# Kernel optimization log

Measured on AMD Instinct MI355X. Metric: run time of the kernel, lower is better.

Reference implementation:

```python
import jax, jax.numpy as jnp
import numpy as np

N_NODES = 100000
N_EDGES = 1600000
N_GRAPHS = 512
IN_CH = 128
FILT = 128
N_CONVS = 4  # 1 + n_rounds(3)


def setup_inputs() -> dict:
    key = jax.random.key(0)
    ks = jax.random.split(key, 10)
    x = jax.random.normal(ks[0], (N_NODES, IN_CH), dtype=jnp.float32)
    edge_index = jax.random.randint(ks[1], (2, N_EDGES), 0, N_NODES, dtype=jnp.int32)
    batch = jnp.sort(jax.random.randint(ks[2], (N_NODES,), 0, N_GRAPHS, dtype=jnp.int32))
    # GCNConv weights (in_channels == filter_size so all convs stack uniformly)
    s = 1.0 / np.sqrt(FILT)
    conv_w = jax.random.uniform(ks[3], (N_CONVS, IN_CH, FILT), jnp.float32, -s, s)
    conv_b = jnp.zeros((N_CONVS, FILT), jnp.float32)
    fc1_w = jax.random.uniform(ks[4], (FILT, FILT), jnp.float32, -s, s)
    fc1_b = jax.random.uniform(ks[5], (FILT,), jnp.float32, -s, s)
    fc2_w = jax.random.uniform(ks[6], (FILT, 1), jnp.float32, -s, s)
    fc2_b = jax.random.uniform(ks[7], (1,), jnp.float32, -s, s)
    return {"x": x, "edge_index": edge_index, "batch": batch, "batch_size": N_GRAPHS,
            "conv_w": conv_w, "conv_b": conv_b,
            "fc1_w": fc1_w, "fc1_b": fc1_b, "fc2_w": fc2_w, "fc2_b": fc2_b}


def _gcn_layer(x, W, b, src, dst, dinv):
    # GCNConv with improved=True: A_hat = A + 2I, sym-normalized by D_hat^{-1/2}
    h = x @ W                                   # [N, F]
    enorm = dinv[src] * dinv[dst]               # [E]
    agg = jax.ops.segment_sum(h[src] * enorm[:, None], dst, num_segments=N_NODES)
    self_loop = (2.0 * dinv * dinv)[:, None] * h
    return agg + self_loop + b


def reference(x, edge_index, batch, batch_size, conv_w, conv_b, fc1_w, fc1_b, fc2_w, fc2_b):
    src, dst = edge_index[0], edge_index[1]
    # degree including improved self-loop weight 2
    deg = jax.ops.segment_sum(jnp.ones((N_EDGES,), x.dtype), dst, num_segments=N_NODES) + 2.0
    dinv = jax.lax.rsqrt(deg)
    for i in range(N_CONVS):
        x = _gcn_layer(x, conv_w[i], conv_b[i], src, dst, dinv)
        x = jax.nn.relu(x)
        # dropout is identity in eval mode
    # global mean pool over graphs
    sums = jax.ops.segment_sum(x, batch, num_segments=batch_size)
    cnt = jax.ops.segment_sum(jnp.ones((N_NODES,), x.dtype), batch, num_segments=batch_size)
    pooled = sums / jnp.maximum(cnt, 1.0)[:, None]   # [G, F]
    h = jax.nn.relu(pooled @ fc1_w + fc1_b)
    out = h @ fc2_w + fc2_b                          # [G, 1]
    return out[:, 0]
```

## Files before the change

### kernel.cpp

```cpp
#include <hip/hip_runtime.h>
#include <hip/hip_fp16.h>

#define N_NODES 100000
#define N_EDGES 1600000
#define N_GRAPHS 512
#define F 128
#define N_CONVS 4
#define SCAN_NBLK ((N_NODES + 1023) / 1024)
#define FILL_BLOCKS ((N_EDGES + 255) / 256)
#define NWIN 8
#define WIN_SZ ((N_NODES + NWIN - 1) / NWIN)

#define W2_STRIDE 132
#define W2_LAYER (128 * W2_STRIDE)

typedef __attribute__((ext_vector_type(8))) short short8;
typedef __attribute__((ext_vector_type(4))) float f32x4;

union FragU { uint4 u; short8 v; };
union HU4 { uint4 u; __half2 h[4]; };

__device__ __forceinline__ float4 fma4(float w, float4 v, float4 a) {
    a.x = fmaf(w, v.x, a.x); a.y = fmaf(w, v.y, a.y);
    a.z = fmaf(w, v.z, a.z); a.w = fmaf(w, v.w, a.w);
    return a;
}

__device__ __forceinline__ unsigned int pack_hilo(float f) {
    unsigned int u = __float_as_uint(f);
    unsigned int hb = u & 0xFFFF0000u;
    float d = f - __uint_as_float(hb);
    unsigned int lb = __float_as_uint(d) >> 16;
    return (u >> 16) | (lb << 16);
}


__global__ void count_kernel(const int* __restrict__ dst, int* __restrict__ cnt) {
    int e = blockIdx.x * blockDim.x + threadIdx.x;
    if (e < N_EDGES) atomicAdd(&cnt[dst[e]], 1);
}

__global__ void dinv_kernel(const int* __restrict__ cnt, float* __restrict__ dinv) {
    int n = blockIdx.x * blockDim.x + threadIdx.x;
    if (n < N_NODES) dinv[n] = rsqrtf((float)cnt[n] + 2.0f);
}

__global__ void scan1_kernel(const int* __restrict__ cnt, int* __restrict__ excl,
                             int* __restrict__ blksum) {
    __shared__ int sums[256];
    int t = threadIdx.x;
    int base = blockIdx.x * 1024 + t * 4;
    int v0 = 0, v1 = 0, v2 = 0, v3 = 0;
    if (base + 0 < N_NODES) v0 = cnt[base + 0];
    if (base + 1 < N_NODES) v1 = cnt[base + 1];
    if (base + 2 < N_NODES) v2 = cnt[base + 2];
    if (base + 3 < N_NODES) v3 = cnt[base + 3];
    int s = v0 + v1 + v2 + v3;
    sums[t] = s;
    __syncthreads();
    for (int off = 1; off < 256; off <<= 1) {
        int y = (t >= off) ? sums[t - off] : 0;
        __syncthreads();
        sums[t] += y;
        __syncthreads();
    }
    int pre = sums[t] - s;
    if (base + 0 < N_NODES) excl[base + 0] = pre;
    if (base + 1 < N_NODES) excl[base + 1] = pre + v0;
    if (base + 2 < N_NODES) excl[base + 2] = pre + v0 + v1;
    if (base + 3 < N_NODES) excl[base + 3] = pre + v0 + v1 + v2;
    if (t == 255) blksum[blockIdx.x] = sums[255];
}

__global__ void scan2_kernel(int* __restrict__ blksum, int nblk) {
    __shared__ int sh[128];
    int t = threadIdx.x;
    int v = (t < nblk) ? blksum[t] : 0;
    sh[t] = v;
    __syncthreads();
    for (int off = 1; off < 128; off <<= 1) {
        int y = (t >= off) ? sh[t - off] : 0;
        __syncthreads();
        sh[t] += y;
        __syncthreads();
    }
    if (t < nblk) blksum[t] = sh[t] - v;
}

__global__ void scan3_kernel(int* __restrict__ rowptr, const int* __restrict__ blksum,
                             int* __restrict__ fill) {
    int t = threadIdx.x;
    int base = blockIdx.x * 1024 + t * 4;
    int off = blksum[blockIdx.x];
#pragma unroll
    for (int i = 0; i < 4; i++) {
        int idx = base + i;
        if (idx < N_NODES) {
            int v = rowptr[idx] + off;
            rowptr[idx] = v;
            fill[idx] = v;
        }
    }
    if (blockIdx.x == 0 && t == 0) rowptr[N_NODES] = N_EDGES;
}


__global__ __launch_bounds__(256) void fillw_kernel(
        const int* __restrict__ src, const int* __restrict__ dst,
        const float* __restrict__ dinv, int* __restrict__ fill,
        int2* __restrict__ edges) {
    int b = blockIdx.x;
    int w = b & (NWIN - 1);
    int e = (b >> 3) * 256 + threadIdx.x;
    if (e < N_EDGES) {
        int d = dst[e];
        if (d / WIN_SZ == w) {
            int s = src[e];
            int pos = atomicAdd(&fill[d], 1);
            edges[pos] = make_int2(s, __float_as_int(dinv[s] * dinv[d]));
        }
    }
}


__global__ void wpack_kernel(const float* __restrict__ conv_w, unsigned int* __restrict__ W2g) {
    int idx = blockIdx.x * 256 + threadIdx.x;
    if (idx < N_CONVS * 16384) {
        int L = idx >> 14;
        int e = idx & 16383;
        int k = e >> 7;
        int n = e & 127;
        float f = conv_w[(size_t)L * 16384 + k * 128 + n];
        W2g[(size_t)L * W2_LAYER + n * W2_STRIDE + k] = pack_hilo(f);
    }
}


__global__ __launch_bounds__(256, 2) void gemm_mfma_kernel(const float* __restrict__ X,
                                                           const unsigned int* __restrict__ W2g,
                                                           __half* __restrict__ Hh) {
    __shared__ unsigned int wlds[128 * W2_STRIDE];
    int t = threadIdx.x;

    {
        const uint4* s4 = (const uint4*)W2g;
        uint4* d4 = (uint4*)wlds;
#pragma unroll
        for (int i = 0; i < 17; i++) {
            int idx = i * 256 + t;
            if (idx < (128 * W2_STRIDE) / 4) d4[idx] = s4[idx];
        }
    }
    __syncthreads();

    int w = t >> 6;
    int l = t & 63;
    int m = l & 15;
    int q = l >> 4;
    int r0 = blockIdx.x * 128 + w * 32 + m;
    int r1 = r0 + 16;
    int r0c = (r0 > N_NODES - 1) ? (N_NODES - 1) : r0;
    int r1c = (r1 > N_NODES - 1) ? (N_NODES - 1) : r1;
    const float4* X4 = (const float4*)X;

    uint4 a0[8], a1[8];
#pragma unroll
    for (int i = 0; i < 8; i++) {
        float4 xv = X4[(size_t)r0c * 32 + i * 4 + q];
        a0[i].x = pack_hilo(xv.x); a0[i].y = pack_hilo(xv.y);
        a0[i].z = pack_hilo(xv.z); a0[i].w = pack_hilo(xv.w);
        float4 yv = X4[(size_t)r1c * 32 + i * 4 + q];
        a1[i].x = pack_hilo(yv.x); a1[i].y = pack_hilo(yv.y);
        a1[i].z = pack_hilo(yv.z); a1[i].w = pack_hilo(yv.w);
    }

    f32x4 acc0[8], acc1[8];
#pragma unroll
    for (int nb = 0; nb < 8; nb++) {
        acc0[nb] = (f32x4){0.f, 0.f, 0.f, 0.f};
        acc1[nb] = (f32x4){0.f, 0.f, 0.f, 0.f};
    }

#pragma unroll
    for (int nb = 0; nb < 8; nb++) {
        const unsigned int* wb = &wlds[(nb * 16 + m) * W2_STRIDE];
#pragma unroll
        for (int i = 0; i < 8; i++) {
            uint4 b = *(const uint4*)(wb + i * 16 + q * 4);
            FragU fa0, fa1, fb, fr;
            fa0.u = a0[i]; fa1.u = a1[i]; fb.u = b;
            acc0[nb] = __builtin_amdgcn_mfma_f32_16x16x32_bf16(fa0.v, fb.v, acc0[nb], 0, 0, 0);
            acc1[nb] = __builtin_amdgcn_mfma_f32_16x16x32_bf16(fa1.v, fb.v, acc1[nb], 0, 0, 0);
            fr.u.x = (b.x >> 16) | (b.x << 16);
            fr.u.y = (b.y >> 16) | (b.y << 16);
            fr.u.z = (b.z >> 16) | (b.z << 16);
            fr.u.w = (b.w >> 16) | (b.w << 16);
            acc0[nb] = __builtin_amdgcn_mfma_f32_16x16x32_bf16(fa0.v, fr.v, acc0[nb], 0, 0, 0);
            acc1[nb] = __builtin_amdgcn_mfma_f32_16x16x32_bf16(fa1.v, fr.v, acc1[nb], 0, 0, 0);
        }
    }

    int rbase = blockIdx.x * 128 + w * 32 + q * 4;
#pragma unroll
    for (int nb = 0; nb < 8; nb++) {
#pragma unroll
        for (int r = 0; r < 4; r++) {
            int row = rbase + r;
            if (row < N_NODES) Hh[(size_t)row * F + nb * 16 + m] = __float2half(acc0[nb][r]);
            int row1 = row + 16;
            if (row1 < N_NODES) Hh[(size_t)row1 * F + nb * 16 + m] = __float2half(acc1[nb][r]);
        }
    }
}


__global__ __launch_bounds__(256) void agg_kernel(const uint4* __restrict__ H16,
                                                  const int* __restrict__ rowptr,
                                                  const int2* __restrict__ edges,
                                                  const float* __restrict__ dinv,
                                                  const float4* __restrict__ bias4,
                                                  float4* __restrict__ Xo4) {
    int node = blockIdx.x * 4 + (threadIdx.x >> 6);
    if (node >= N_NODES) return;
    int lane = threadIdx.x & 63;
    int c16 = lane & 15;
    int slot = lane >> 4;

    int lo = rowptr[node];
    int hi = rowptr[node + 1];
    int him1 = hi - 1;

    float4 aL = make_float4(0.f, 0.f, 0.f, 0.f);
    float4 aH = make_float4(0.f, 0.f, 0.f, 0.f);

    for (int i = lo + slot; i < hi; i += 16) {
        int s[4]; float w[4]; uint4 v[4];
#pragma unroll
        for (int j = 0; j < 4; j++) {
            int ij = i + 4 * j;
            int cj = (ij < him1) ? ij : him1;
            int2 e = edges[cj];
            s[j] = e.x;
            w[j] = (ij < hi) ? __int_as_float(e.y) : 0.f;
        }
#pragma unroll
        for (int j = 0; j < 4; j++) v[j] = H16[(size_t)s[j] * 16 + c16];
#pragma unroll
        for (int j = 0; j < 4; j++) {
            HU4 x; x.u = v[j];
            float2 p0 = __half22float2(x.h[0]);
            float2 p1 = __half22float2(x.h[1]);
            float2 p2 = __half22float2(x.h[2]);
            float2 p3 = __half22float2(x.h[3]);
            aL.x = fmaf(w[j], p0.x, aL.x); aL.y = fmaf(w[j], p0.y, aL.y);
            aL.z = fmaf(w[j], p1.x, aL.z); aL.w = fmaf(w[j], p1.y, aL.w);
            aH.x = fmaf(w[j], p2.x, aH.x); aH.y = fmaf(w[j], p2.y, aH.y);
            aH.z = fmaf(w[j], p3.x, aH.z); aH.w = fmaf(w[j], p3.y, aH.w);
        }
    }

    aL.x += __shfl_down(aL.x, 32, 64); aL.y += __shfl_down(aL.y, 32, 64);
    aL.z += __shfl_down(aL.z, 32, 64); aL.w += __shfl_down(aL.w, 32, 64);
    aH.x += __shfl_down(aH.x, 32, 64); aH.y += __shfl_down(aH.y, 32, 64);
    aH.z += __shfl_down(aH.z, 32, 64); aH.w += __shfl_down(aH.w, 32, 64);
    aL.x += __shfl_down(aL.x, 16, 64); aL.y += __shfl_down(aL.y, 16, 64);
    aL.z += __shfl_down(aL.z, 16, 64); aL.w += __shfl_down(aL.w, 16, 64);
    aH.x += __shfl_down(aH.x, 16, 64); aH.y += __shfl_down(aH.y, 16, 64);
    aH.z += __shfl_down(aH.z, 16, 64); aH.w += __shfl_down(aH.w, 16, 64);

    if (slot == 0) {
        float dn = dinv[node];
        float sw = 2.0f * dn * dn;
        HU4 x; x.u = H16[(size_t)node * 16 + c16];
        float2 p0 = __half22float2(x.h[0]);
        float2 p1 = __half22float2(x.h[1]);
        float2 p2 = __half22float2(x.h[2]);
        float2 p3 = __half22float2(x.h[3]);
        float4 bL = bias4[c16 * 2];
        float4 bH = bias4[c16 * 2 + 1];
        float4 rL, rH;
        rL.x = fmaxf(fmaf(sw, p0.x, aL.x) + bL.x, 0.f);
        rL.y = fmaxf(fmaf(sw, p0.y, aL.y) + bL.y, 0.f);
        rL.z = fmaxf(fmaf(sw, p1.x, aL.z) + bL.z, 0.f);
        rL.w = fmaxf(fmaf(sw, p1.y, aL.w) + bL.w, 0.f);
        rH.x = fmaxf(fmaf(sw, p2.x, aH.x) + bH.x, 0.f);
        rH.y = fmaxf(fmaf(sw, p2.y, aH.y) + bH.y, 0.f);
        rH.z = fmaxf(fmaf(sw, p3.x, aH.z) + bH.z, 0.f);
        rH.w = fmaxf(fmaf(sw, p3.y, aH.w) + bH.w, 0.f);
        Xo4[(size_t)node * 32 + c16 * 2]     = rL;
        Xo4[(size_t)node * 32 + c16 * 2 + 1] = rH;
    }
}


__global__ __launch_bounds__(256) void pool_fc_kernel(const float* __restrict__ x,
                                                      const int* __restrict__ batch,
                                                      const float* __restrict__ fc1w,
                                                      const float* __restrict__ fc1b,
                                                      const float* __restrict__ fc2w,
                                                      const float* __restrict__ fc2b,
                                                      float* __restrict__ out) {
    __shared__ float part[2][F];
    __shared__ float pooled[F];
    __shared__ int bnd[2];
    __shared__ float red[2];
    int g = blockIdx.x, t = threadIdx.x;
    int c = t & 127, hlf = t >> 7;

    if (t < 2) {
        int target = g + t;
        int lo = 0, hi = N_NODES;
        while (lo < hi) {
            int m = (lo + hi) >> 1;
            if (batch[m] < target) lo = m + 1;
            else hi = m;
        }
        bnd[t] = lo;
    }
    __syncthreads();
    int lo = bnd[0], hi = bnd[1];

    float s = 0.f;
    int n = lo + hlf;
    for (; n + 6 < hi; n += 8) {
        float v0 = x[(size_t)n * F + c];
        float v1 = x[(size_t)(n + 2) * F + c];
        float v2 = x[(size_t)(n + 4) * F + c];
        float v3 = x[(size_t)(n + 6) * F + c];
        s += (v0 + v1) + (v2 + v3);
    }
    for (; n < hi; n += 2) s += x[(size_t)n * F + c];
    part[hlf][c] = s;
    __syncthreads();

    if (t < F) {
        float cntf = fmaxf((float)(hi - lo), 1.0f);
        pooled[c] = (part[0][c] + part[1][c]) / cntf;
    }
    __syncthreads();

    if (t < F) {
        float acc = fc1b[t];
#pragma unroll 4
        for (int k = 0; k < F; k++) acc = fmaf(pooled[k], fc1w[k * F + t], acc);
        acc = fmaxf(acc, 0.f);

        float p = acc * fc2w[t];
#pragma unroll
        for (int o = 32; o > 0; o >>= 1) p += __shfl_down(p, o, 64);
        if ((t & 63) == 0) red[t >> 6] = p;
    }
    __syncthreads();
    if (t == 0) out[g] = red[0] + red[1] + fc2b[0];
}


extern "C" void kernel_launch(void* const* d_in, const int* in_sizes, int n_in,
                              void* d_out, int out_size, void* d_ws, size_t ws_size,
                              hipStream_t stream) {
    const float* x_in   = (const float*)d_in[0];
    const int*   eidx   = (const int*)d_in[1];
    const int*   batch  = (const int*)d_in[2];
    const float* conv_w = (const float*)d_in[4];
    const float* conv_b = (const float*)d_in[5];
    const float* fc1w   = (const float*)d_in[6];
    const float* fc1b   = (const float*)d_in[7];
    const float* fc2w   = (const float*)d_in[8];
    const float* fc2b   = (const float*)d_in[9];
    float* out = (float*)d_out;

    const int* src = eidx;
    const int* dst = eidx + N_EDGES;

    char* ws = (char*)d_ws;
    size_t off = 0;
    auto alloc = [&](size_t bytes) -> char* {
        char* p = ws + off;
        off += (bytes + 255) & ~(size_t)255;
        return p;
    };
    float*  bufA  = (float*)alloc((size_t)N_NODES * F * 4);
    __half* bufH  = (__half*)alloc((size_t)N_NODES * F * 2);
    float*  dinv  = (float*)alloc((size_t)N_NODES * 4);
    int*    cnt   = (int*)alloc((size_t)N_NODES * 4);
    int*    rowp  = (int*)alloc((size_t)(N_NODES + 1) * 4);
    int*    fill  = (int*)alloc((size_t)N_NODES * 4);
    int2*   edges = (int2*)alloc((size_t)N_EDGES * 8);
    unsigned int* W2g = (unsigned int*)alloc((size_t)N_CONVS * W2_LAYER * 4);
    int*    blks  = (int*)alloc(128 * 4);
    (void)ws_size; (void)in_sizes; (void)n_in; (void)out_size;

    hipMemsetAsync(cnt, 0, (size_t)N_NODES * 4, stream);
    count_kernel<<<(N_EDGES + 255) / 256, 256, 0, stream>>>(dst, cnt);
    dinv_kernel<<<(N_NODES + 255) / 256, 256, 0, stream>>>(cnt, dinv);
    scan1_kernel<<<SCAN_NBLK, 256, 0, stream>>>(cnt, rowp, blks);
    scan2_kernel<<<1, 128, 0, stream>>>(blks, SCAN_NBLK);
    scan3_kernel<<<SCAN_NBLK, 256, 0, stream>>>(rowp, blks, fill);
    wpack_kernel<<<(N_CONVS * 16384 + 255) / 256, 256, 0, stream>>>(conv_w, W2g);

    fillw_kernel<<<FILL_BLOCKS * NWIN, 256, 0, stream>>>(src, dst, dinv, fill, edges);

    const float* cur = x_in;
    for (int L = 0; L < N_CONVS; L++) {
        gemm_mfma_kernel<<<(N_NODES + 127) / 128, 256, 0, stream>>>(
            cur, W2g + (size_t)L * W2_LAYER, bufH);
        agg_kernel<<<(N_NODES + 3) / 4, 256, 0, stream>>>(
            (const uint4*)bufH, rowp, edges, dinv,
            (const float4*)(conv_b + (size_t)L * F), (float4*)bufA);
        cur = bufA;
    }

    pool_fc_kernel<<<N_GRAPHS, 256, 0, stream>>>(bufA, batch, fc1w, fc1b, fc2w, fc2b, out);
}
```

Measured before the change: 635.6 us.

## Store layer activations in fp16 and aggregate two nodes per wavefront

Intermediate layer outputs are now written as fp16 instead of fp32. This halves the bytes the aggregation kernel writes and the next GEMM and pooling kernels read, and a new fp16-input GEMM variant consumes them. The aggregation kernel also processes two destination nodes per wavefront with interleaved gathers, giving more memory-level parallelism and half as many blocks. The trade-offs are fp16 rounding of activations and imbalance when the two nodes have different degrees.

```diff
diff --git a/kernel.cpp b/kernel.cpp
--- a/kernel.cpp
+++ b/kernel.cpp
@@ -18,13 +18,8 @@
 typedef __attribute__((ext_vector_type(4))) float f32x4;
 
 union FragU { uint4 u; short8 v; };
+union HU { uint2 u; __half2 h[2]; };
 union HU4 { uint4 u; __half2 h[4]; };
-
-__device__ __forceinline__ float4 fma4(float w, float4 v, float4 a) {
-    a.x = fmaf(w, v.x, a.x); a.y = fmaf(w, v.y, a.y);
-    a.z = fmaf(w, v.z, a.z); a.w = fmaf(w, v.w, a.w);
-    return a;
-}
 
 __device__ __forceinline__ unsigned int pack_hilo(float f) {
     unsigned int u = __float_as_uint(f);
@@ -32,6 +27,14 @@
     float d = f - __uint_as_float(hb);
     unsigned int lb = __float_as_uint(d) >> 16;
     return (u >> 16) | (lb << 16);
+}
+
+__device__ __forceinline__ float4 red4(float4 a) {
+    a.x += __shfl_down(a.x, 32, 64); a.y += __shfl_down(a.y, 32, 64);
+    a.z += __shfl_down(a.z, 32, 64); a.w += __shfl_down(a.w, 32, 64);
+    a.x += __shfl_down(a.x, 16, 64); a.y += __shfl_down(a.y, 16, 64);
+    a.z += __shfl_down(a.z, 16, 64); a.w += __shfl_down(a.w, 16, 64);
+    return a;
 }
 
 
@@ -136,81 +139,101 @@
 }
 
 
-__global__ __launch_bounds__(256, 2) void gemm_mfma_kernel(const float* __restrict__ X,
-                                                           const unsigned int* __restrict__ W2g,
-                                                           __half* __restrict__ Hh) {
-    __shared__ unsigned int wlds[128 * W2_STRIDE];
-    int t = threadIdx.x;
-
-    {
-        const uint4* s4 = (const uint4*)W2g;
-        uint4* d4 = (uint4*)wlds;
-#pragma unroll
-        for (int i = 0; i < 17; i++) {
-            int idx = i * 256 + t;
-            if (idx < (128 * W2_STRIDE) / 4) d4[idx] = s4[idx];
-        }
-    }
-    __syncthreads();
-
-    int w = t >> 6;
-    int l = t & 63;
-    int m = l & 15;
-    int q = l >> 4;
-    int r0 = blockIdx.x * 128 + w * 32 + m;
-    int r1 = r0 + 16;
-    int r0c = (r0 > N_NODES - 1) ? (N_NODES - 1) : r0;
-    int r1c = (r1 > N_NODES - 1) ? (N_NODES - 1) : r1;
-    const float4* X4 = (const float4*)X;
-
-    uint4 a0[8], a1[8];
-#pragma unroll
-    for (int i = 0; i < 8; i++) {
-        float4 xv = X4[(size_t)r0c * 32 + i * 4 + q];
-        a0[i].x = pack_hilo(xv.x); a0[i].y = pack_hilo(xv.y);
-        a0[i].z = pack_hilo(xv.z); a0[i].w = pack_hilo(xv.w);
-        float4 yv = X4[(size_t)r1c * 32 + i * 4 + q];
-        a1[i].x = pack_hilo(yv.x); a1[i].y = pack_hilo(yv.y);
-        a1[i].z = pack_hilo(yv.z); a1[i].w = pack_hilo(yv.w);
-    }
-
-    f32x4 acc0[8], acc1[8];
-#pragma unroll
-    for (int nb = 0; nb < 8; nb++) {
-        acc0[nb] = (f32x4){0.f, 0.f, 0.f, 0.f};
-        acc1[nb] = (f32x4){0.f, 0.f, 0.f, 0.f};
-    }
-
-#pragma unroll
-    for (int nb = 0; nb < 8; nb++) {
-        const unsigned int* wb = &wlds[(nb * 16 + m) * W2_STRIDE];
-#pragma unroll
+#define GEMM_BODY(LOAD_AFRAGS)                                                      \
+    __shared__ unsigned int wlds[128 * W2_STRIDE];                                  \
+    int t = threadIdx.x;                                                            \
+    {                                                                               \
+        const uint4* s4 = (const uint4*)W2g;                                        \
+        uint4* d4 = (uint4*)wlds;                                                   \
+        _Pragma("unroll")                                                           \
+        for (int i = 0; i < 17; i++) {                                              \
+            int idx = i * 256 + t;                                                  \
+            if (idx < (128 * W2_STRIDE) / 4) d4[idx] = s4[idx];                     \
+        }                                                                           \
+    }                                                                               \
+    __syncthreads();                                                                \
+    int w = t >> 6;                                                                 \
+    int l = t & 63;                                                                 \
+    int m = l & 15;                                                                 \
+    int q = l >> 4;                                                                 \
+    int r0 = blockIdx.x * 128 + w * 32 + m;                                         \
+    int r1 = r0 + 16;                                                               \
+    int r0c = (r0 > N_NODES - 1) ? (N_NODES - 1) : r0;                              \
+    int r1c = (r1 > N_NODES - 1) ? (N_NODES - 1) : r1;                              \
+    uint4 a0[8], a1[8];                                                             \
+    LOAD_AFRAGS                                                                     \
+    f32x4 acc0[8], acc1[8];                                                         \
+    _Pragma("unroll")                                                               \
+    for (int nb = 0; nb < 8; nb++) {                                                \
+        acc0[nb] = (f32x4){0.f, 0.f, 0.f, 0.f};                                     \
+        acc1[nb] = (f32x4){0.f, 0.f, 0.f, 0.f};                                     \
+    }                                                                               \
+    _Pragma("unroll")                                                               \
+    for (int nb = 0; nb < 8; nb++) {                                                \
+        const unsigned int* wb = &wlds[(nb * 16 + m) * W2_STRIDE];                  \
+        _Pragma("unroll")                                                           \
+        for (int i = 0; i < 8; i++) {                                               \
+            uint4 b = *(const uint4*)(wb + i * 16 + q * 4);                         \
+            FragU fa0, fa1, fb, fr;                                                 \
+            fa0.u = a0[i]; fa1.u = a1[i]; fb.u = b;                                 \
+            acc0[nb] = __builtin_amdgcn_mfma_f32_16x16x32_bf16(fa0.v, fb.v, acc0[nb], 0, 0, 0); \
+            acc1[nb] = __builtin_amdgcn_mfma_f32_16x16x32_bf16(fa1.v, fb.v, acc1[nb], 0, 0, 0); \
+            fr.u.x = (b.x >> 16) | (b.x << 16);                                     \
+            fr.u.y = (b.y >> 16) | (b.y << 16);                                     \
+            fr.u.z = (b.z >> 16) | (b.z << 16);                                     \
+            fr.u.w = (b.w >> 16) | (b.w << 16);                                     \
+            acc0[nb] = __builtin_amdgcn_mfma_f32_16x16x32_bf16(fa0.v, fr.v, acc0[nb], 0, 0, 0); \
+            acc1[nb] = __builtin_amdgcn_mfma_f32_16x16x32_bf16(fa1.v, fr.v, acc1[nb], 0, 0, 0); \
+        }                                                                           \
+    }                                                                               \
+    int rbase = blockIdx.x * 128 + w * 32 + q * 4;                                  \
+    _Pragma("unroll")                                                               \
+    for (int nb = 0; nb < 8; nb++) {                                                \
+        _Pragma("unroll")                                                           \
+        for (int r = 0; r < 4; r++) {                                               \
+            int row = rbase + r;                                                    \
+            if (row < N_NODES) Hh[(size_t)row * F + nb * 16 + m] = __float2half(acc0[nb][r]); \
+            int row1 = row + 16;                                                    \
+            if (row1 < N_NODES) Hh[(size_t)row1 * F + nb * 16 + m] = __float2half(acc1[nb][r]); \
+        }                                                                           \
+    }
+
+__global__ __launch_bounds__(256, 2) void gemm_mfma_f32(const float* __restrict__ X,
+                                                        const unsigned int* __restrict__ W2g,
+                                                        __half* __restrict__ Hh) {
+    GEMM_BODY(
+        const float4* X4 = (const float4*)X;
+        _Pragma("unroll")
         for (int i = 0; i < 8; i++) {
-            uint4 b = *(const uint4*)(wb + i * 16 + q * 4);
-            FragU fa0, fa1, fb, fr;
-            fa0.u = a0[i]; fa1.u = a1[i]; fb.u = b;
-            acc0[nb] = __builtin_amdgcn_mfma_f32_16x16x32_bf16(fa0.v, fb.v, acc0[nb], 0, 0, 0);
-            acc1[nb] = __builtin_amdgcn_mfma_f32_16x16x32_bf16(fa1.v, fb.v, acc1[nb], 0, 0, 0);
-            fr.u.x = (b.x >> 16) | (b.x << 16);
-            fr.u.y = (b.y >> 16) | (b.y << 16);
-            fr.u.z = (b.z >> 16) | (b.z << 16);
-            fr.u.w = (b.w >> 16) | (b.w << 16);
-            acc0[nb] = __builtin_amdgcn_mfma_f32_16x16x32_bf16(fa0.v, fr.v, acc0[nb], 0, 0, 0);
-            acc1[nb] = __builtin_amdgcn_mfma_f32_16x16x32_bf16(fa1.v, fr.v, acc1[nb], 0, 0, 0);
-        }
-    }
-
-    int rbase = blockIdx.x * 128 + w * 32 + q * 4;
-#pragma unroll
-    for (int nb = 0; nb < 8; nb++) {
-#pragma unroll
-        for (int r = 0; r < 4; r++) {
-            int row = rbase + r;
-            if (row < N_NODES) Hh[(size_t)row * F + nb * 16 + m] = __float2half(acc0[nb][r]);
-            int row1 = row + 16;
-            if (row1 < N_NODES) Hh[(size_t)row1 * F + nb * 16 + m] = __float2half(acc1[nb][r]);
-        }
-    }
+            float4 xv = X4[(size_t)r0c * 32 + i * 4 + q];
+            a0[i].x = pack_hilo(xv.x); a0[i].y = pack_hilo(xv.y);
+            a0[i].z = pack_hilo(xv.z); a0[i].w = pack_hilo(xv.w);
+            float4 yv = X4[(size_t)r1c * 32 + i * 4 + q];
+            a1[i].x = pack_hilo(yv.x); a1[i].y = pack_hilo(yv.y);
+            a1[i].z = pack_hilo(yv.z); a1[i].w = pack_hilo(yv.w);
+        }
+    )
+}
+
+__global__ __launch_bounds__(256, 2) void gemm_mfma_f16(const __half* __restrict__ X,
+                                                        const unsigned int* __restrict__ W2g,
+                                                        __half* __restrict__ Hh) {
+    GEMM_BODY(
+        const uint2* Xh = (const uint2*)X;
+        _Pragma("unroll")
+        for (int i = 0; i < 8; i++) {
+            HU hu0; hu0.u = Xh[(size_t)r0c * 32 + i * 4 + q];
+            float2 f01 = __half22float2(hu0.h[0]);
+            float2 f23 = __half22float2(hu0.h[1]);
+            a0[i].x = pack_hilo(f01.x); a0[i].y = pack_hilo(f01.y);
+            a0[i].z = pack_hilo(f23.x); a0[i].w = pack_hilo(f23.y);
+            HU hu1; hu1.u = Xh[(size_t)r1c * 32 + i * 4 + q];
+            float2 g01 = __half22float2(hu1.h[0]);
+            float2 g23 = __half22float2(hu1.h[1]);
+            a1[i].x = pack_hilo(g01.x); a1[i].y = pack_hilo(g01.y);
+            a1[i].z = pack_hilo(g23.x); a1[i].w = pack_hilo(g23.y);
+        }
+    )
 }
 
 
@@ -219,81 +242,113 @@
                                                   const int2* __restrict__ edges,
                                                   const float* __restrict__ dinv,
                                                   const float4* __restrict__ bias4,
-                                                  float4* __restrict__ Xo4) {
-    int node = blockIdx.x * 4 + (threadIdx.x >> 6);
-    if (node >= N_NODES) return;
+                                                  uint4* __restrict__ Xo16) {
+    int wv = threadIdx.x >> 6;
+    int nodeA = blockIdx.x * 8 + wv * 2;
+    int nodeB = nodeA + 1;
     int lane = threadIdx.x & 63;
     int c16 = lane & 15;
     int slot = lane >> 4;
 
-    int lo = rowptr[node];
-    int hi = rowptr[node + 1];
-    int him1 = hi - 1;
-
-    float4 aL = make_float4(0.f, 0.f, 0.f, 0.f);
-    float4 aH = make_float4(0.f, 0.f, 0.f, 0.f);
-
-    for (int i = lo + slot; i < hi; i += 16) {
-        int s[4]; float w[4]; uint4 v[4];
+    int nA = (nodeA > N_NODES - 1) ? (N_NODES - 1) : nodeA;
+    int nB = (nodeB > N_NODES - 1) ? (N_NODES - 1) : nodeB;
+    int loA = rowptr[nA], hiA = rowptr[nA + 1];
+    int loB = rowptr[nB], hiB = rowptr[nB + 1];
+    int hA1 = hiA - 1; if (hA1 < 0) hA1 = 0;
+    int hB1 = hiB - 1; if (hB1 < 0) hB1 = 0;
+
+    float4 aAL = make_float4(0.f, 0.f, 0.f, 0.f), aAH = aAL;
+    float4 aBL = aAL, aBH = aAL;
+
+    int iA = loA + slot, iB = loB + slot;
+    while (iA < hiA || iB < hiB) {
+        int sA[4], sB[4]; float wA[4], wB[4]; uint4 vA[4], vB[4];
 #pragma unroll
         for (int j = 0; j < 4; j++) {
-            int ij = i + 4 * j;
-            int cj = (ij < him1) ? ij : him1;
-            int2 e = edges[cj];
-            s[j] = e.x;
-            w[j] = (ij < hi) ? __int_as_float(e.y) : 0.f;
-        }
-#pragma unroll
-        for (int j = 0; j < 4; j++) v[j] = H16[(size_t)s[j] * 16 + c16];
+            int ija = iA + 4 * j;
+            int cja = (ija < hA1) ? ija : hA1;
+            int2 eA = edges[cja];
+            sA[j] = eA.x; wA[j] = (ija < hiA) ? __int_as_float(eA.y) : 0.f;
+            int ijb = iB + 4 * j;
+            int cjb = (ijb < hB1) ? ijb : hB1;
+            int2 eB = edges[cjb];
+            sB[j] = eB.x; wB[j] = (ijb < hiB) ? __int_as_float(eB.y) : 0.f;
+        }
 #pragma unroll
         for (int j = 0; j < 4; j++) {
-            HU4 x; x.u = v[j];
+            vA[j] = H16[(size_t)sA[j] * 16 + c16];
+            vB[j] = H16[(size_t)sB[j] * 16 + c16];
+        }
+#pragma unroll
+        for (int j = 0; j < 4; j++) {
+            HU4 x; float2 p0, p1, p2, p3;
+            x.u = vA[j];
+            p0 = __half22float2(x.h[0]); p1 = __half22float2(x.h[1]);
+            p2 = __half22float2(x.h[2]); p3 = __half22float2(x.h[3]);
+            aAL.x = fmaf(wA[j], p0.x, aAL.x); aAL.y = fmaf(wA[j], p0.y, aAL.y);
+            aAL.z = fmaf(wA[j], p1.x, aAL.z); aAL.w = fmaf(wA[j], p1.y, aAL.w);
+            aAH.x = fmaf(wA[j], p2.x, aAH.x); aAH.y = fmaf(wA[j], p2.y, aAH.y);
+            aAH.z = fmaf(wA[j], p3.x, aAH.z); aAH.w = fmaf(wA[j], p3.y, aAH.w);
+            x.u = vB[j];
+            p0 = __half22float2(x.h[0]); p1 = __half22float2(x.h[1]);
+            p2 = __half22float2(x.h[2]); p3 = __half22float2(x.h[3]);
+            aBL.x = fmaf(wB[j], p0.x, aBL.x); aBL.y = fmaf(wB[j], p0.y, aBL.y);
+            aBL.z = fmaf(wB[j], p1.x, aBL.z); aBL.w = fmaf(wB[j], p1.y, aBL.w);
+            aBH.x = fmaf(wB[j], p2.x, aBH.x); aBH.y = fmaf(wB[j], p2.y, aBH.y);
+            aBH.z = fmaf(wB[j], p3.x, aBH.z); aBH.w = fmaf(wB[j], p3.y, aBH.w);
+        }
+        iA += 16; iB += 16;
+    }
+
+    aAL = red4(aAL); aAH = red4(aAH);
+    aBL = red4(aBL); aBH = red4(aBH);
+
+    if (slot == 0) {
+        float4 bL = bias4[c16 * 2];
+        float4 bH = bias4[c16 * 2 + 1];
+        if (nodeA < N_NODES) {
+            float dn = dinv[nodeA];
+            float sw = 2.0f * dn * dn;
+            HU4 x; x.u = H16[(size_t)nodeA * 16 + c16];
             float2 p0 = __half22float2(x.h[0]);
             float2 p1 = __half22float2(x.h[1]);
             float2 p2 = __half22float2(x.h[2]);
             float2 p3 = __half22float2(x.h[3]);
-            aL.x = fmaf(w[j], p0.x, aL.x); aL.y = fmaf(w[j], p0.y, aL.y);
-            aL.z = fmaf(w[j], p1.x, aL.z); aL.w = fmaf(w[j], p1.y, aL.w);
-            aH.x = fmaf(w[j], p2.x, aH.x); aH.y = fmaf(w[j], p2.y, aH.y);
-            aH.z = fmaf(w[j], p3.x, aH.z); aH.w = fmaf(w[j], p3.y, aH.w);
-        }
-    }
-
-    aL.x += __shfl_down(aL.x, 32, 64); aL.y += __shfl_down(aL.y, 32, 64);
-    aL.z += __shfl_down(aL.z, 32, 64); aL.w += __shfl_down(aL.w, 32, 64);
-    aH.x += __shfl_down(aH.x, 32, 64); aH.y += __shfl_down(aH.y, 32, 64);
-    aH.z += __shfl_down(aH.z, 32, 64); aH.w += __shfl_down(aH.w, 32, 64);
-    aL.x += __shfl_down(aL.x, 16, 64); aL.y += __shfl_down(aL.y, 16, 64);
-    aL.z += __shfl_down(aL.z, 16, 64); aL.w += __shfl_down(aL.w, 16, 64);
-    aH.x += __shfl_down(aH.x, 16, 64); aH.y += __shfl_down(aH.y, 16, 64);
-    aH.z += __shfl_down(aH.z, 16, 64); aH.w += __shfl_down(aH.w, 16, 64);
-
-    if (slot == 0) {
-        float dn = dinv[node];
-        float sw = 2.0f * dn * dn;
-        HU4 x; x.u = H16[(size_t)node * 16 + c16];
-        float2 p0 = __half22float2(x.h[0]);
-        float2 p1 = __half22float2(x.h[1]);
-        float2 p2 = __half22float2(x.h[2]);
-        float2 p3 = __half22float2(x.h[3]);
-        float4 bL = bias4[c16 * 2];
-        float4 bH = bias4[c16 * 2 + 1];
-        float4 rL, rH;
-        rL.x = fmaxf(fmaf(sw, p0.x, aL.x) + bL.x, 0.f);
-        rL.y = fmaxf(fmaf(sw, p0.y, aL.y) + bL.y, 0.f);
-        rL.z = fmaxf(fmaf(sw, p1.x, aL.z) + bL.z, 0.f);
-        rL.w = fmaxf(fmaf(sw, p1.y, aL.w) + bL.w, 0.f);
-        rH.x = fmaxf(fmaf(sw, p2.x, aH.x) + bH.x, 0.f);
-        rH.y = fmaxf(fmaf(sw, p2.y, aH.y) + bH.y, 0.f);
-        rH.z = fmaxf(fmaf(sw, p3.x, aH.z) + bH.z, 0.f);
-        rH.w = fmaxf(fmaf(sw, p3.y, aH.w) + bH.w, 0.f);
-        Xo4[(size_t)node * 32 + c16 * 2]     = rL;
-        Xo4[(size_t)node * 32 + c16 * 2 + 1] = rH;
-    }
-}
-
-
-__global__ __launch_bounds__(256) void pool_fc_kernel(const float* __restrict__ x,
+            HU4 o;
+            o.h[0] = __floats2half2_rn(fmaxf(fmaf(sw, p0.x, aAL.x) + bL.x, 0.f),
+                                       fmaxf(fmaf(sw, p0.y, aAL.y) + bL.y, 0.f));
+            o.h[1] = __floats2half2_rn(fmaxf(fmaf(sw, p1.x, aAL.z) + bL.z, 0.f),
+                                       fmaxf(fmaf(sw, p1.y, aAL.w) + bL.w, 0.f));
+            o.h[2] = __floats2half2_rn(fmaxf(fmaf(sw, p2.x, aAH.x) + bH.x, 0.f),
+                                       fmaxf(fmaf(sw, p2.y, aAH.y) + bH.y, 0.f));
+            o.h[3] = __floats2half2_rn(fmaxf(fmaf(sw, p3.x, aAH.z) + bH.z, 0.f),
+                                       fmaxf(fmaf(sw, p3.y, aAH.w) + bH.w, 0.f));
+            Xo16[(size_t)nodeA * 16 + c16] = o.u;
+        }
+        if (nodeB < N_NODES) {
+            float dn = dinv[nodeB];
+            float sw = 2.0f * dn * dn;
+            HU4 x; x.u = H16[(size_t)nodeB * 16 + c16];
+            float2 p0 = __half22float2(x.h[0]);
+            float2 p1 = __half22float2(x.h[1]);
+            float2 p2 = __half22float2(x.h[2]);
+            float2 p3 = __half22float2(x.h[3]);
+            HU4 o;
+            o.h[0] = __floats2half2_rn(fmaxf(fmaf(sw, p0.x, aBL.x) + bL.x, 0.f),
+                                       fmaxf(fmaf(sw, p0.y, aBL.y) + bL.y, 0.f));
+            o.h[1] = __floats2half2_rn(fmaxf(fmaf(sw, p1.x, aBL.z) + bL.z, 0.f),
+                                       fmaxf(fmaf(sw, p1.y, aBL.w) + bL.w, 0.f));
+            o.h[2] = __floats2half2_rn(fmaxf(fmaf(sw, p2.x, aBH.x) + bH.x, 0.f),
+                                       fmaxf(fmaf(sw, p2.y, aBH.y) + bH.y, 0.f));
+            o.h[3] = __floats2half2_rn(fmaxf(fmaf(sw, p3.x, aBH.z) + bH.z, 0.f),
+                                       fmaxf(fmaf(sw, p3.y, aBH.w) + bH.w, 0.f));
+            Xo16[(size_t)nodeB * 16 + c16] = o.u;
+        }
+    }
+}
+
+
+__global__ __launch_bounds__(256) void pool_fc_kernel(const __half* __restrict__ x,
                                                       const int* __restrict__ batch,
                                                       const float* __restrict__ fc1w,
                                                       const float* __restrict__ fc1b,
@@ -323,13 +378,13 @@
     float s = 0.f;
     int n = lo + hlf;
     for (; n + 6 < hi; n += 8) {
-        float v0 = x[(size_t)n * F + c];
-        float v1 = x[(size_t)(n + 2) * F + c];
-        float v2 = x[(size_t)(n + 4) * F + c];
-        float v3 = x[(size_t)(n + 6) * F + c];
+        float v0 = __half2float(x[(size_t)n * F + c]);
+        float v1 = __half2float(x[(size_t)(n + 2) * F + c]);
+        float v2 = __half2float(x[(size_t)(n + 4) * F + c]);
+        float v3 = __half2float(x[(size_t)(n + 6) * F + c]);
         s += (v0 + v1) + (v2 + v3);
     }
-    for (; n < hi; n += 2) s += x[(size_t)n * F + c];
+    for (; n < hi; n += 2) s += __half2float(x[(size_t)n * F + c]);
     part[hlf][c] = s;
     __syncthreads();
 
@@ -379,7 +434,7 @@
         off += (bytes + 255) & ~(size_t)255;
         return p;
     };
-    float*  bufA  = (float*)alloc((size_t)N_NODES * F * 4);
+    __half* bufX  = (__half*)alloc((size_t)N_NODES * F * 2);
     __half* bufH  = (__half*)alloc((size_t)N_NODES * F * 2);
     float*  dinv  = (float*)alloc((size_t)N_NODES * 4);
     int*    cnt   = (int*)alloc((size_t)N_NODES * 4);
@@ -400,15 +455,17 @@
 
     fillw_kernel<<<FILL_BLOCKS * NWIN, 256, 0, stream>>>(src, dst, dinv, fill, edges);
 
-    const float* cur = x_in;
-    for (int L = 0; L < N_CONVS; L++) {
-        gemm_mfma_kernel<<<(N_NODES + 127) / 128, 256, 0, stream>>>(
-            cur, W2g + (size_t)L * W2_LAYER, bufH);
-        agg_kernel<<<(N_NODES + 3) / 4, 256, 0, stream>>>(
+    gemm_mfma_f32<<<(N_NODES + 127) / 128, 256, 0, stream>>>(x_in, W2g, bufH);
+    agg_kernel<<<(N_NODES + 7) / 8, 256, 0, stream>>>(
+        (const uint4*)bufH, rowp, edges, dinv,
+        (const float4*)conv_b, (uint4*)bufX);
+    for (int L = 1; L < N_CONVS; L++) {
+        gemm_mfma_f16<<<(N_NODES + 127) / 128, 256, 0, stream>>>(
+            bufX, W2g + (size_t)L * W2_LAYER, bufH);
+        agg_kernel<<<(N_NODES + 7) / 8, 256, 0, stream>>>(
             (const uint4*)bufH, rowp, edges, dinv,
-            (const float4*)(conv_b + (size_t)L * F), (float4*)bufA);
-        cur = bufA;
-    }
-
-    pool_fc_kernel<<<N_GRAPHS, 256, 0, stream>>>(bufA, batch, fc1w, fc1b, fc2w, fc2b, out);
-}
+            (const float4*)(conv_b + (size_t)L * F), (uint4*)bufX);
+    }
+
+    pool_fc_kernel<<<N_GRAPHS, 256, 0, stream>>>(bufX, batch, fc1w, fc1b, fc2w, fc2b, out);
+}
```

Result: no change. 637.9 us (+0.4%).
